# Kernel tuning notes

Measured on AMD Instinct MI355X. Metric: run time of the kernel, lower is better.

The kernel has to match this reference:

```python
import jax, jax.numpy as jnp
import numpy as np

DIM, HEADS, HD, TOPK, SCALE = 256, 8, 32, 4, 2


def _conv1x1(x, w, b):
    # 1x1 Conv2d with folded (eval-mode) BatchNorm -> affine: weight (O,C), bias (O,)
    return jnp.einsum('bchw,oc->bohw', x, w) + b[None, :, None, None]


def setup_inputs() -> dict:
    key = jax.random.key(0)
    ks = jax.random.split(key, 12)
    b, h, w = 2, 64, 64
    hu, wu = 32, 32
    s = lambda fan: 1.0 / np.sqrt(fan)
    return {
        'x': jax.random.normal(ks[0], (b, DIM, h, w), jnp.float32),
        'upper_feat': jax.random.normal(ks[1], (b, DIM, hu, wu), jnp.float32),
        'q_w': jax.random.normal(ks[2], (DIM, DIM), jnp.float32) * s(DIM),
        'q_b': jnp.zeros((DIM,), jnp.float32),
        'kv_w': jax.random.normal(ks[3], (2 * DIM, DIM), jnp.float32) * s(DIM),
        'kv_b': jnp.zeros((2 * DIM,), jnp.float32),
        'proj_w': jax.random.normal(ks[4], (DIM, DIM), jnp.float32) * s(DIM),
        'proj_b': jnp.zeros((DIM,), jnp.float32),
        'pe_w': jax.random.normal(ks[5], (DIM, 1, 7, 7), jnp.float32) * s(49),
        'pe_b': jnp.zeros((DIM,), jnp.float32),
        'gate_w': jax.random.normal(ks[6], (HD, 2 * HD), jnp.float32) * s(2 * HD),
        'gate_b': jnp.zeros((HD,), jnp.float32),
    }


def reference(x, upper_feat, q_w, q_b, kv_w, kv_b, proj_w, proj_b, pe_w, pe_b, gate_w, gate_b):
    b, c, h, w = x.shape
    n = h * w
    _, _, hu, wu = upper_feat.shape
    nu = hu * wu
    # projections -> (b, H, seq, d)
    q = _conv1x1(x, q_w, q_b).reshape(b, HEADS, HD, n).transpose(0, 1, 3, 2)
    kv = _conv1x1(upper_feat, kv_w, kv_b).reshape(b, HEADS, 2 * HD, nu).transpose(0, 1, 3, 2)
    k, v = kv[..., :HD], kv[..., HD:]
    # coarse cross-attention (fine queries -> coarse keys)
    sim = jnp.einsum('bhnd,bhmd->bhnm', q, k) * (HD ** -0.5)  # [b,H,n,nu]
    attn = jax.nn.softmax(sim, axis=-1)
    coarse = jnp.einsum('bhnm,bhmd->bhnd', attn, v)
    # fine branch: gumbel top-k over coarse positions, gather 2x2 fine blocks
    f_kv = _conv1x1(x, kv_w, kv_b).reshape(b, HEADS, 2 * HD, n).transpose(0, 1, 3, 2)
    f_k, f_v = f_kv[..., :HD], f_kv[..., HD:]
    gsim = sim.mean(axis=2)  # [b,H,nu]
    gum = jax.random.gumbel(jax.random.key(42), gsim.shape, gsim.dtype)
    soft = jax.nn.softmax(gsim + gum, axis=-1)
    _, ti = jax.lax.top_k(soft, TOPK)  # [b,H,k]
    h_idx = (ti // wu) * SCALE
    w_idx = (ti % wu) * SCALE
    txi = jnp.concatenate([(h_idx + dh) * w + (w_idx + dw)
                           for dh in range(SCALE) for dw in range(SCALE)], axis=-1)  # [b,H,4k]
    tk = jnp.take_along_axis(f_k, txi[..., None], axis=2)  # [b,H,4k,d]
    tv = jnp.take_along_axis(f_v, txi[..., None], axis=2)
    fine = jax.nn.softmax(jnp.einsum('bhnd,bhmd->bhnm', q, tk) * (HD ** -0.5), axis=-1)
    refined = jnp.einsum('bhnm,bhmd->bhnd', fine, tv)
    # gated fusion (Conv1d kernel_size=1 == linear over channels, shared across heads)
    fus = jnp.concatenate([coarse, refined], axis=-1)  # [b,H,n,2d]
    gate = jax.nn.sigmoid(jnp.einsum('bhnc,dc->bhnd', fus, gate_w) + gate_b)
    x_out = gate * refined + (1.0 - gate) * coarse
    x_out = x_out.transpose(0, 1, 3, 2).reshape(b, c, h, w)
    # depthwise 7x7 conv PE on coarse V, upsampled bilinearly (align_corners=False)
    v_r = v.transpose(0, 1, 3, 2).reshape(b, c, hu, wu)
    v_pe = jax.lax.conv_general_dilated(
        v_r, pe_w, window_strides=(1, 1), padding=((3, 3), (3, 3)),
        dimension_numbers=('NCHW', 'OIHW', 'NCHW'), feature_group_count=c)
    v_pe = v_pe + pe_b[None, :, None, None]
    v_pe = jax.image.resize(v_pe, (b, c, h, w), method='bilinear')
    return _conv1x1(x_out + v_pe, proj_w, proj_b)
```

## Files before the change

kernel.cpp:

```cpp
#include <hip/hip_runtime.h>
#include <cstdint>
#include <cstddef>

#define SCALE_F 0.17677669529663687f
#define SHIFT_F 8.0f

typedef __bf16 bf16x8 __attribute__((ext_vector_type(8)));
typedef float  floatx4 __attribute__((ext_vector_type(4)));
#define MFMA16(a,b,c) __builtin_amdgcn_mfma_f32_16x16x32_bf16(a, b, c, 0, 0, 0)

__device__ __forceinline__ unsigned short f2bf(float x) {
  unsigned u = __float_as_uint(x);
  u += 0x7FFFu + ((u >> 16) & 1u);
  return (unsigned short)(u >> 16);
}
__device__ __forceinline__ float bf2f(unsigned short h) {
  return __uint_as_float((unsigned)h << 16);
}
union bfu { unsigned short u; __bf16 b; };
__device__ __forceinline__ __bf16 us2bf(unsigned short u) { bfu t; t.u = u; return t.b; }
__device__ __forceinline__ void bfsplit(float x, unsigned short& h, unsigned short& l) {
  h = f2bf(x);
  l = f2bf(x - bf2f(h));
}
__device__ __forceinline__ unsigned cvt_pk_bf16(float lo, float hi) {
  unsigned r;
  asm("v_cvt_pk_bf16_f32 %0, %1, %2" : "=v"(r) : "v"(lo), "v"(hi));
  return r;
}
__device__ __forceinline__ void bfsplit2(float a, float b,
                                         unsigned& h2, unsigned& l2) {
  h2 = cvt_pk_bf16(a, b);
  float ra = a - __uint_as_float(h2 << 16);
  float rb = b - __uint_as_float(h2 & 0xffff0000u);
  l2 = cvt_pk_bf16(ra, rb);
}

__device__ __forceinline__ unsigned rotl32(unsigned v, int d) {
  return (v << d) | (v >> (32 - d));
}

__device__ __forceinline__ void threefry2x32(unsigned k0, unsigned k1,
                                             unsigned& x0, unsigned& x1) {
  unsigned k2 = k0 ^ k1 ^ 0x1BD11BDAu;
  x0 += k0; x1 += k1;
#define TF_R(r) { x0 += x1; x1 = rotl32(x1, r); x1 ^= x0; }
  TF_R(13) TF_R(15) TF_R(26) TF_R(6)
  x0 += k1; x1 += k2 + 1u;
  TF_R(17) TF_R(29) TF_R(16) TF_R(24)
  x0 += k2; x1 += k0 + 2u;
  TF_R(13) TF_R(15) TF_R(26) TF_R(6)
  x0 += k0; x1 += k1 + 3u;
  TF_R(17) TF_R(29) TF_R(16) TF_R(24)
  x0 += k1; x1 += k2 + 4u;
  TF_R(13) TF_R(15) TF_R(26) TF_R(6)
  x0 += k2; x1 += k0 + 5u;
#undef TF_R
}

__device__ __forceinline__ float jax_gumbel_key42(unsigned idx) {
  unsigned x0 = 0u, x1 = idx;
  threefry2x32(0u, 42u, x0, x1);
  unsigned bits = x0 ^ x1;
  unsigned fb = (bits >> 9) | 0x3f800000u;
  float f = __uint_as_float(fb) - 1.0f;
  const float tiny = 1.17549435e-38f;
  float u = f * (1.0f - tiny) + tiny;
  u = fmaxf(tiny, u);
  return -logf(-logf(u));
}

__device__ __forceinline__ float quad_xor1_add(float x) {
  int v = __builtin_amdgcn_mov_dpp(__float_as_int(x), 0xB1, 0xF, 0xF, true);
  return x + __int_as_float(v);
}
__device__ __forceinline__ float quad_xor2_add(float x) {
  int v = __builtin_amdgcn_mov_dpp(__float_as_int(x), 0x4E, 0xF, 0xF, true);
  return x + __int_as_float(v);
}

template<int MODE>
__device__ __forceinline__ void convmf_body(
    int bx, int by, int bz,
    const float* __restrict__ W, const float* __restrict__ bias,
    const float* __restrict__ X, float* __restrict__ Y,
    const float* __restrict__ vpe, float* __restrict__ qbar_g,
    unsigned short* __restrict__ bhs, unsigned short* __restrict__ bls) {
  const int tid  = threadIdx.x;
  const int lane = tid & 63;
  const int w    = tid >> 6;
  const int col  = lane & 15;
  const int quad = lane >> 4;
  const int sn0 = (tid & 15) * 4;
  const int sc0 = (tid >> 4) * 2;

  float wy0 = 0.f, wy1 = 0.f; int r0 = 0, r1 = 0;
  float wx0[4], wx1[4]; int cl0[4], cl1[4];
  if constexpr (MODE == 1) {
    float sy = 0.5f * (float)bx - 0.25f;
    int fy = (int)floorf(sy);
    wy1 = sy - (float)fy; wy0 = 1.0f - wy1;
    r0 = fy < 0 ? 0 : fy; r1 = (fy + 1) > 31 ? 31 : (fy + 1);
    #pragma unroll
    for (int k = 0; k < 4; ++k) {
      int jc = sn0 + k;
      float sx = 0.5f * (float)jc - 0.25f;
      int fx = (int)floorf(sx);
      wx1[k] = sx - (float)fx; wx0[k] = 1.0f - wx1[k];
      cl0[k] = fx < 0 ? 0 : fx; cl1[k] = (fx + 1) > 31 ? 31 : (fx + 1);
    }
  }

  const float* Xb = X + (size_t)bz * 256 * 4096 + bx * 64;

  bf16x8 wah[8], wal[8];
  {
    const float* wrow = W + (size_t)(by*64 + w*16 + col) * 256;
    #pragma unroll
    for (int s = 0; s < 8; ++s) {
      #pragma unroll
      for (int t = 0; t < 4; ++t) {
        float wa = wrow[s*32 + quad*8 + 2*t];
        float wb = wrow[s*32 + quad*8 + 2*t + 1];
        unsigned h2, l2;
        bfsplit2(wa, wb, h2, l2);
        ((unsigned*)&wah[s])[t] = h2;
        ((unsigned*)&wal[s])[t] = l2;
      }
    }
  }

  floatx4 f[4] = {{0.f,0.f,0.f,0.f},{0.f,0.f,0.f,0.f},{0.f,0.f,0.f,0.f},{0.f,0.f,0.f,0.f}};

  #pragma unroll
  for (int h2i = 0; h2i < 2; ++h2i) {
    #pragma unroll
    for (int s4 = 0; s4 < 4; ++s4) {
      int c = h2i*128 + s4*32 + sc0;
      int cl_ = c - h2i*128;
      float4 xa = *(const float4*)(Xb + (size_t)c * 4096 + sn0);
      float4 xb = *(const float4*)(Xb + (size_t)(c + 1) * 4096 + sn0);
      float ea[4] = {xa.x, xa.y, xa.z, xa.w};
      float eb[4] = {xb.x, xb.y, xb.z, xb.w};
      if constexpr (MODE == 1) {
        const float* vpa = vpe + ((size_t)bz * 256 + c) * 1024;
        const float* vpb = vpa + 1024;
        #pragma unroll
        for (int i = 0; i < 4; ++i) {
          ea[i] += wy0 * (wx0[i]*vpa[r0*32 + cl0[i]] + wx1[i]*vpa[r0*32 + cl1[i]])
                 + wy1 * (wx0[i]*vpa[r1*32 + cl0[i]] + wx1[i]*vpa[r1*32 + cl1[i]]);
          eb[i] += wy0 * (wx0[i]*vpb[r0*32 + cl0[i]] + wx1[i]*vpb[r0*32 + cl1[i]])
                 + wy1 * (wx0[i]*vpb[r1*32 + cl0[i]] + wx1[i]*vpb[r1*32 + cl1[i]]);
        }
      }
      #pragma unroll
      for (int i = 0; i < 4; ++i) {
        unsigned h2, l2;
        bfsplit2(ea[i], eb[i], h2, l2);
        *(unsigned*)(bhs + (sn0 + i) * 136 + cl_) = h2;
        *(unsigned*)(bls + (sn0 + i) * 136 + cl_) = l2;
      }
    }
    __syncthreads();

    #pragma unroll
    for (int sl = 0; sl < 4; ++sl) {
      int s = h2i*4 + sl;
      #pragma unroll
      for (int nt = 0; nt < 4; ++nt) {
        bf16x8 bh8 = *(const bf16x8*)(bhs + (nt*16 + col)*136 + sl*32 + quad*8);
        bf16x8 bl8 = *(const bf16x8*)(bls + (nt*16 + col)*136 + sl*32 + quad*8);
        f[nt] = MFMA16(wah[s], bh8, f[nt]);
        f[nt] = MFMA16(wal[s], bh8, f[nt]);
        f[nt] = MFMA16(wah[s], bl8, f[nt]);
      }
    }
    __syncthreads();
  }

  float* Yb = Y + (size_t)bz * 256 * 4096 + bx * 64;
  #pragma unroll
  for (int r = 0; r < 4; ++r) {
    int o = by*64 + w*16 + quad*4 + r;
    float bi = bias[o];
    float rs = 0.f;
    #pragma unroll
    for (int nt = 0; nt < 4; ++nt) {
      float val = f[nt][r] + bi;
      Yb[(size_t)o*4096 + nt*16 + col] = val;
      rs += val;
    }
    if constexpr (MODE == 0) {
      rs += __shfl_xor(rs, 1); rs += __shfl_xor(rs, 2);
      rs += __shfl_xor(rs, 4); rs += __shfl_xor(rs, 8);
      if (col == 0) atomicAdd(qbar_g + bz*256 + o, rs);
    }
  }
}

__device__ __forceinline__ void convkv_body(
    int bx, int by, int bz,
    const float* __restrict__ W, const float* __restrict__ bias,
    const float* __restrict__ X, float* __restrict__ Y,
    float* __restrict__ Y2,
    unsigned short* __restrict__ KH, unsigned short* __restrict__ KL,
    unsigned short* __restrict__ VH, unsigned short* __restrict__ VL,
    float (*As)[68], float (*Bs)[68]) {
  const int tid = threadIdx.x;
  const int tx = tid & 15, ty = tid >> 4;
  const int C = 256, N = 1024;
  const float* Xb = X + (size_t)bz * C * N + bx * 64;
  const int ar = tid >> 2;
  const int ac = (tid & 3) * 4;
  const int bc = tid >> 4;
  const int bn = (tid & 15) * 4;
  float acc[4][4] = {};

  for (int kc = 0; kc < C; kc += 32) {
    float4 av0 = *(const float4*)(W + (size_t)(by * 64 + ar) * C + kc + ac);
    float4 av1 = *(const float4*)(W + (size_t)(by * 64 + ar) * C + kc + 16 + ac);
    float4 bv0 = *(const float4*)(Xb + (size_t)(kc + bc) * N + bn);
    float4 bv1 = *(const float4*)(Xb + (size_t)(kc + 16 + bc) * N + bn);
    As[ac+0][ar]  = av0.x; As[ac+1][ar]  = av0.y; As[ac+2][ar]  = av0.z; As[ac+3][ar]  = av0.w;
    As[ac+16][ar] = av1.x; As[ac+17][ar] = av1.y; As[ac+18][ar] = av1.z; As[ac+19][ar] = av1.w;
    *(float4*)&Bs[bc][bn]      = bv0;
    *(float4*)&Bs[bc + 16][bn] = bv1;
    __syncthreads();
    #pragma unroll 8
    for (int kk = 0; kk < 32; ++kk) {
      float4 a = *(const float4*)&As[kk][ty*4];
      float4 b = *(const float4*)&Bs[kk][tx*4];
      acc[0][0] = fmaf(a.x, b.x, acc[0][0]); acc[0][1] = fmaf(a.x, b.y, acc[0][1]);
      acc[0][2] = fmaf(a.x, b.z, acc[0][2]); acc[0][3] = fmaf(a.x, b.w, acc[0][3]);
      acc[1][0] = fmaf(a.y, b.x, acc[1][0]); acc[1][1] = fmaf(a.y, b.y, acc[1][1]);
      acc[1][2] = fmaf(a.y, b.z, acc[1][2]); acc[1][3] = fmaf(a.y, b.w, acc[1][3]);
      acc[2][0] = fmaf(a.z, b.x, acc[2][0]); acc[2][1] = fmaf(a.z, b.y, acc[2][1]);
      acc[2][2] = fmaf(a.z, b.z, acc[2][2]); acc[2][3] = fmaf(a.z, b.w, acc[2][3]);
      acc[3][0] = fmaf(a.w, b.x, acc[3][0]); acc[3][1] = fmaf(a.w, b.y, acc[3][1]);
      acc[3][2] = fmaf(a.w, b.z, acc[3][2]); acc[3][3] = fmaf(a.w, b.w, acc[3][3]);
    }
    __syncthreads();
  }

  float vals[4][4];
  #pragma unroll
  for (int i = 0; i < 4; ++i) {
    float bi = bias[by*64 + ty*4 + i];
    #pragma unroll
    for (int j = 0; j < 4; ++j) vals[i][j] = acc[i][j] + bi;
  }

  #pragma unroll
  for (int i = 0; i < 4; ++i) {
    int o = by*64 + ty*4 + i;
    int hh = o >> 6, dd = o & 63;
    float* yb = Y + (size_t)bz*524288 + (size_t)hh*65536 + dd;
    #pragma unroll
    for (int j = 0; j < 4; ++j) {
      int m = bx*64 + tx*4 + j;
      yb[(size_t)m*64] = vals[i][j];
      if (dd >= 32)
        Y2[((size_t)bz*256 + hh*32 + (dd-32))*1024 + m] = vals[i][j];
    }
  }
  const int bh_ = bz*8 + by;
  const int dd0 = ty*4;
  if (dd0 < 32) {
    #pragma unroll
    for (int j = 0; j < 4; ++j) {
      int m = bx*64 + tx*4 + j;
      uint2 ph, pl;
      bfsplit2(vals[0][j], vals[1][j], ph.x, pl.x);
      bfsplit2(vals[2][j], vals[3][j], ph.y, pl.y);
      *(uint2*)(KH + ((size_t)bh_*1024 + m)*32 + dd0) = ph;
      *(uint2*)(KL + ((size_t)bh_*1024 + m)*32 + dd0) = pl;
    }
  } else {
    const int m0 = bx*64 + tx*4;
    const int ml = (m0 >> 2) & 7;
    const int mp = (m0 & ~31) + ((ml & 3) << 3) + ((ml >> 2) << 2);
    #pragma unroll
    for (int i = 0; i < 4; ++i) {
      int dv = dd0 + i - 32;
      uint2 ph, pl;
      bfsplit2(vals[i][0], vals[i][1], ph.x, pl.x);
      bfsplit2(vals[i][2], vals[i][3], ph.y, pl.y);
      *(uint2*)(VH + ((size_t)bh_*32 + dv)*1024 + mp) = ph;
      *(uint2*)(VL + ((size_t)bh_*32 + dv)*1024 + mp) = pl;
    }
  }
}

__global__ __launch_bounds__(256)
void front_kernel(const float* __restrict__ q_w, const float* __restrict__ q_b,
                  const float* __restrict__ x, float* __restrict__ q_cm,
                  float* __restrict__ qbar_g,
                  const float* __restrict__ kv_w, const float* __restrict__ kv_b,
                  const float* __restrict__ upper,
                  float* __restrict__ kv_m, float* __restrict__ v_ch,
                  unsigned short* __restrict__ KH, unsigned short* __restrict__ KL,
                  unsigned short* __restrict__ VH, unsigned short* __restrict__ VL) {
  __shared__ __align__(16) char fsm[34816];
  if (blockIdx.x < 256) {
    int idx = blockIdx.x;
    convkv_body(idx & 15, (idx >> 4) & 7, idx >> 7,
                kv_w, kv_b, upper, kv_m, v_ch, KH, KL, VH, VL,
                (float(*)[68])fsm, (float(*)[68])(fsm + 8704));
  } else {
    int idx = blockIdx.x - 256;
    convmf_body<0>(idx & 63, (idx >> 6) & 3, idx >> 8,
                   q_w, q_b, x, q_cm, nullptr, qbar_g,
                   (unsigned short*)fsm, (unsigned short*)(fsm + 17408));
  }
}

__global__ __launch_bounds__(256)
void mid_kernel(const float* __restrict__ qbar_g, const float* __restrict__ kv_m,
                const float* __restrict__ x, const float* __restrict__ kv_w,
                const float* __restrict__ kv_b, float* __restrict__ fkv_g,
                const float* __restrict__ v_ch, const float* __restrict__ pe_w,
                const float* __restrict__ pe_b, float* __restrict__ v_pe) {
  __shared__ float qbar[32];
  __shared__ float vals[1024];
  __shared__ float rv[256];
  __shared__ int ri[256];
  __shared__ int txi_s[16];
  __shared__ float xcol[16][260];
  __shared__ float vch[1024];
  __shared__ float wch[49];
  const int tid = threadIdx.x;

  if (blockIdx.x < 64) {
    const int bh = blockIdx.x >> 2;
    const int quarter = blockIdx.x & 3;
    const int b = bh >> 3, hh = bh & 7;

    if (tid < 32) qbar[tid] = qbar_g[b*256 + hh*32 + tid] * (1.0f/4096.0f);
    __syncthreads();

    for (int m = tid; m < 1024; m += 256) {
      const float* kbp = kv_m + (size_t)bh*65536 + (size_t)m*64;
      float s = 0.f;
      #pragma unroll
      for (int d4 = 0; d4 < 8; ++d4) {
        float4 kk = *(const float4*)&kbp[d4*4];
        s = fmaf(qbar[d4*4+0], kk.x, s);
        s = fmaf(qbar[d4*4+1], kk.y, s);
        s = fmaf(qbar[d4*4+2], kk.z, s);
        s = fmaf(qbar[d4*4+3], kk.w, s);
      }
      vals[m] = s * SCALE_F + jax_gumbel_key42((unsigned)(bh*1024 + m));
    }
    __syncthreads();

    int sel[4];
    for (int t = 0; t < 4; ++t) {
      float bv = -INFINITY; int bi = 0x7fffffff;
      for (int m = tid; m < 1024; m += 256) {
        float v = vals[m];
        if (v > bv || (v == bv && m < bi)) { bv = v; bi = m; }
      }
      rv[tid] = bv; ri[tid] = bi;
      __syncthreads();
      for (int st = 128; st >= 1; st >>= 1) {
        if (tid < st) {
          float ov = rv[tid+st]; int oi = ri[tid+st];
          if (ov > rv[tid] || (ov == rv[tid] && oi < ri[tid])) { rv[tid] = ov; ri[tid] = oi; }
        }
        __syncthreads();
      }
      int w = ri[0];
      sel[t] = w;
      __syncthreads();
      if (tid == 0) vals[w] = -INFINITY;
      __syncthreads();
    }

    if (tid == 0) {
      #pragma unroll
      for (int t = 0; t < 4; ++t) {
        int ti = sel[t];
        int hi = (ti >> 5) * 2, wi = (ti & 31) * 2;
        #pragma unroll
        for (int dh = 0; dh < 2; ++dh)
          #pragma unroll
          for (int dw = 0; dw < 2; ++dw)
            txi_s[(dh*2+dw)*4 + t] = (hi+dh)*64 + (wi+dw);
      }
    }
    __syncthreads();

    #pragma unroll
    for (int i = 0; i < 16; ++i) {
      int e = tid + 256*i;
      int c = e >> 4, j = e & 15;
      xcol[j][c] = x[(size_t)b*1048576 + (size_t)c*4096 + txi_s[j]];
    }
    __syncthreads();
    const int dd = quarter*16 + (tid >> 4);
    const int j  = tid & 15;
    const int o  = hh*64 + dd;
    const float* wrow = kv_w + (size_t)o*256;
    float a0 = 0.f, a1 = 0.f, a2 = 0.f, a3 = 0.f;
    const float* xc = &xcol[j][0];
    #pragma unroll 4
    for (int c = 0; c < 256; c += 4) {
      a0 = fmaf(wrow[c+0], xc[c+0], a0);
      a1 = fmaf(wrow[c+1], xc[c+1], a1);
      a2 = fmaf(wrow[c+2], xc[c+2], a2);
      a3 = fmaf(wrow[c+3], xc[c+3], a3);
    }
    fkv_g[(size_t)bh*1024 + dd*16 + j] = ((a0+a1)+(a2+a3)) + kv_b[o];
  } else {
    const int bc = blockIdx.x - 64;
    const int b = bc >> 8, c = bc & 255;
    const float* src = v_ch + ((size_t)b*256 + c)*1024;
    #pragma unroll
    for (int i = 0; i < 4; ++i) vch[tid + 256*i] = src[tid + 256*i];
    if (tid < 49) wch[tid] = pe_w[c*49 + tid];
    float pb = pe_b[c];
    __syncthreads();
    #pragma unroll
    for (int pi = 0; pi < 4; ++pi) {
      int p = tid + 256*pi;
      int i0 = p >> 5, j0 = p & 31;
      float s = 0.f;
      #pragma unroll
      for (int ky = 0; ky < 7; ++ky) {
        int yy = i0 + ky - 3;
        if (yy < 0 || yy > 31) continue;
        #pragma unroll
        for (int kx = 0; kx < 7; ++kx) {
          int xx = j0 + kx - 3;
          if (xx < 0 || xx > 31) continue;
          s = fmaf(wch[ky*7+kx], vch[yy*32+xx], s);
        }
      }
      v_pe[((size_t)b*256 + c)*1024 + p] = s + pb;
    }
  }
}

__global__ __launch_bounds__(256)
void proj_kernel(const float* __restrict__ proj_w, const float* __restrict__ proj_b,
                 const float* __restrict__ x_o, float* __restrict__ out,
                 const float* __restrict__ vpe) {
  __shared__ __align__(16) char fsm[34816];
  convmf_body<1>(blockIdx.x, blockIdx.y, blockIdx.z,
                 proj_w, proj_b, x_o, out, vpe, nullptr,
                 (unsigned short*)fsm, (unsigned short*)(fsm + 17408));
}

__global__ __launch_bounds__(512, 2)
void attn_kernel(const float* __restrict__ q_cm,
                 const unsigned short* __restrict__ kb_h,
                 const unsigned short* __restrict__ kb_l,
                 const unsigned short* __restrict__ vb_h,
                 const unsigned short* __restrict__ vb_l,
                 const float* __restrict__ fkv_g,
                 const float* __restrict__ gate_w, const float* __restrict__ gate_b,
                 float* __restrict__ x_o) {
  __shared__ __align__(16) char smem[48256];
  float* gw_s = (float*)smem;
  float* gb_s = (float*)(smem + 9216);
  float* tk   = (float*)(smem + 9344);
  float* tv   = (float*)(smem + 11392);
  char*  region = smem + 13440;

  const int tid  = threadIdx.x;
  const int lane = tid & 63;
  const int w    = tid >> 6;
  const int qpair = w & 3;
  const int half  = w >> 2;
  const int col  = lane & 15;
  const int quad = lane >> 4;

  const int linear = blockIdx.y * 32 + blockIdx.x;
  const int xcd  = linear & 7;
  const int slot = linear >> 3;
  const int bh = xcd * 2 + (slot >> 5);
  const int nx = slot & 31;
  const int b = bh >> 3, hh = bh & 7;
  const int n0 = nx * 128;

  #pragma unroll
  for (int i = 0; i < 4; ++i) {
    int e = tid + 512*i;
    gw_s[(e >> 6)*72 + (e & 63)] = gate_w[e];
  }
  if (tid < 32) gb_s[tid] = gate_b[tid];

  if (tid < 256) {
    const float* src = fkv_g + (size_t)bh * 1024;
    #pragma unroll
    for (int i = 0; i < 4; ++i) {
      int e4 = (tid & 63) + 64 * i;
      float4 val = ((const float4*)src)[e4];
      int e = e4 * 4;
      int dd = e >> 4, j0 = e & 15;
      float* dst = (dd < 32) ? tk : tv;
      int ddv = (dd < 32) ? dd : dd - 32;
      dst[(j0+0)*32 + ddv] = val.x;
      dst[(j0+1)*32 + ddv] = val.y;
      dst[(j0+2)*32 + ddv] = val.z;
      dst[(j0+3)*32 + ddv] = val.w;
    }
  }
  __syncthreads();

  const float* qbase_cm = q_cm + ((size_t)b*256 + hh*32)*4096 + n0;
  const int qf = tid >> 2;
  const int sf = tid & 3;

  bf16x8 aqh0, aql0, aqh1, aql1;
  #pragma unroll
  for (int j = 0; j < 8; ++j) {
    float qv0 = qbase_cm[(size_t)(quad*8 + j)*4096 + qpair*32 + col];
    float qv1 = qbase_cm[(size_t)(quad*8 + j)*4096 + qpair*32 + 16 + col];
    unsigned short h, l;
    bfsplit(qv0, h, l);
    aqh0[j] = us2bf(h); aql0[j] = us2bf(l);
    bfsplit(qv1, h, l);
    aqh1[j] = us2bf(h); aql1[j] = us2bf(l);
  }

  const unsigned short* kph = kb_h + (size_t)bh * 32768;
  const unsigned short* kpl = kb_l + (size_t)bh * 32768;
  const unsigned short* vph = vb_h + (size_t)bh * 32768;
  const unsigned short* vpl = vb_l + (size_t)bh * 32768;
  const int mbase = half * 512;

#define LDKH(c, t) (*(const bf16x8*)(kph + ((size_t)(mbase + (c)*32 + (t)*16 + col))*32 + quad*8))
#define LDKL(c, t) (*(const bf16x8*)(kpl + ((size_t)(mbase + (c)*32 + (t)*16 + col))*32 + quad*8))
#define LDVH(c, t) (*(const bf16x8*)(vph + ((size_t)((t)*16 + col))*1024 + mbase + (c)*32 + quad*8))
#define LDVL(c, t) (*(const bf16x8*)(vpl + ((size_t)((t)*16 + col))*1024 + mbase + (c)*32 + quad*8))

  floatx4 oA0 = {0.f,0.f,0.f,0.f}, oA1 = {0.f,0.f,0.f,0.f};
  floatx4 oB0 = {0.f,0.f,0.f,0.f}, oB1 = {0.f,0.f,0.f,0.f};
  const floatx4 zero = {0.f, 0.f, 0.f, 0.f};
  float lsA = 0.f, lsB = 0.f;

  floatx4 sA0, sA1, sB0, sB1;
  {
    bf16x8 k0h = LDKH(0,0), k1h = LDKH(0,1);
    bf16x8 k0l = LDKL(0,0), k1l = LDKL(0,1);
    sA0 = MFMA16(k0h, aqh0, zero); sA0 = MFMA16(k0h, aql0, sA0); sA0 = MFMA16(k0l, aqh0, sA0);
    sA1 = MFMA16(k1h, aqh0, zero); sA1 = MFMA16(k1h, aql0, sA1); sA1 = MFMA16(k1l, aqh0, sA1);
    sB0 = MFMA16(k0h, aqh1, zero); sB0 = MFMA16(k0h, aql1, sB0); sB0 = MFMA16(k0l, aqh1, sB0);
    sB1 = MFMA16(k1h, aqh1, zero); sB1 = MFMA16(k1h, aql1, sB1); sB1 = MFMA16(k1l, aqh1, sB1);
  }

  for (int c = 0; c < 16; ++c) {
    bf16x8 v0h = LDVH(c,0), v1h = LDVH(c,1);
    bf16x8 v0l = LDVL(c,0), v1l = LDVL(c,1);
    bf16x8 nk0h, nk1h, nk0l, nk1l;
    if (c < 15) {
      nk0h = LDKH(c+1,0); nk1h = LDKH(c+1,1);
      nk0l = LDKL(c+1,0); nk1l = LDKL(c+1,1);
    }

    float pA0[4], pA1[4], pB0[4], pB1[4];
    #pragma unroll
    for (int r = 0; r < 4; ++r) {
      pA0[r] = __expf(fmaf(sA0[r], SCALE_F, -SHIFT_F));
      pA1[r] = __expf(fmaf(sA1[r], SCALE_F, -SHIFT_F));
      pB0[r] = __expf(fmaf(sB0[r], SCALE_F, -SHIFT_F));
      pB1[r] = __expf(fmaf(sB1[r], SCALE_F, -SHIFT_F));
      lsA += pA0[r] + pA1[r];
      lsB += pB0[r] + pB1[r];
    }
    bf16x8 paA, paB;
    ((unsigned*)&paA)[0] = cvt_pk_bf16(pA0[0], pA0[1]);
    ((unsigned*)&paA)[1] = cvt_pk_bf16(pA0[2], pA0[3]);
    ((unsigned*)&paA)[2] = cvt_pk_bf16(pA1[0], pA1[1]);
    ((unsigned*)&paA)[3] = cvt_pk_bf16(pA1[2], pA1[3]);
    ((unsigned*)&paB)[0] = cvt_pk_bf16(pB0[0], pB0[1]);
    ((unsigned*)&paB)[1] = cvt_pk_bf16(pB0[2], pB0[3]);
    ((unsigned*)&paB)[2] = cvt_pk_bf16(pB1[0], pB1[1]);
    ((unsigned*)&paB)[3] = cvt_pk_bf16(pB1[2], pB1[3]);

    oA0 = MFMA16(paA, v0h, oA0); oA0 = MFMA16(paA, v0l, oA0);
    oA1 = MFMA16(paA, v1h, oA1); oA1 = MFMA16(paA, v1l, oA1);
    oB0 = MFMA16(paB, v0h, oB0); oB0 = MFMA16(paB, v0l, oB0);
    oB1 = MFMA16(paB, v1h, oB1); oB1 = MFMA16(paB, v1l, oB1);

    if (c < 15) {
      sA0 = MFMA16(nk0h, aqh0, zero); sA0 = MFMA16(nk0h, aql0, sA0); sA0 = MFMA16(nk0l, aqh0, sA0);
      sA1 = MFMA16(nk1h, aqh0, zero); sA1 = MFMA16(nk1h, aql0, sA1); sA1 = MFMA16(nk1l, aqh0, sA1);
      sB0 = MFMA16(nk0h, aqh1, zero); sB0 = MFMA16(nk0h, aql1, sB0); sB0 = MFMA16(nk0l, aqh1, sB0);
      sB1 = MFMA16(nk1h, aqh1, zero); sB1 = MFMA16(nk1h, aql1, sB1); sB1 = MFMA16(nk1l, aqh1, sB1);
    }
  }
#undef LDKH
#undef LDKL
#undef LDVH
#undef LDVL

  lsA += __shfl_xor(lsA, 16); lsA += __shfl_xor(lsA, 32);
  lsB += __shfl_xor(lsB, 16); lsB += __shfl_xor(lsB, 32);

  {
    float* cacc = (float*)region;
    float* cl   = (float*)region + 8448;
    #pragma unroll
    for (int r = 0; r < 4; ++r) {
      int qa = qpair*32 + quad*4 + r;
      cacc[(half*128 + qa)*33 + col]      = oA0[r];
      cacc[(half*128 + qa)*33 + 16 + col] = oA1[r];
      int qb = qa + 16;
      cacc[(half*128 + qb)*33 + col]      = oB0[r];
      cacc[(half*128 + qb)*33 + 16 + col] = oB1[r];
    }
    if (quad == 0) {
      cl[half*128 + qpair*32 + col]      = lsA;
      cl[half*128 + qpair*32 + 16 + col] = lsB;
    }
  }

  float rfn[8];
  float crs[8];
  {
    float qfv[8];
    #pragma unroll
    for (int j = 0; j < 8; ++j)
      qfv[j] = qbase_cm[(size_t)(sf + 4*j)*4096 + qf];
    float p16[16]; float fl = 0.f;
    #pragma unroll
    for (int k = 0; k < 16; ++k) {
      const float* kr = tk + k*32 + sf;
      float tp = qfv[0]*kr[0];
      tp = fmaf(qfv[1], kr[4], tp);  tp = fmaf(qfv[2], kr[8], tp);
      tp = fmaf(qfv[3], kr[12], tp); tp = fmaf(qfv[4], kr[16], tp);
      tp = fmaf(qfv[5], kr[20], tp); tp = fmaf(qfv[6], kr[24], tp);
      tp = fmaf(qfv[7], kr[28], tp);
      float full = quad_xor2_add(quad_xor1_add(tp));
      float e = __expf(fmaf(full, SCALE_F, -SHIFT_F));
      p16[k] = e; fl += e;
    }
    float finv = 1.0f / fl;
    #pragma unroll
    for (int j = 0; j < 8; ++j) {
      float r = 0.f;
      #pragma unroll
      for (int k = 0; k < 16; ++k) r = fmaf(p16[k], tv[k*32 + sf + 4*j], r);
      rfn[j] = r * finv;
    }
  }
  __syncthreads();

  {
    const float* cacc = (const float*)region;
    const float* cl   = (const float*)region + 8448;
    float lt = cl[qf] + cl[128 + qf];
    float cinv = 1.0f / lt;
    #pragma unroll
    for (int j = 0; j < 8; ++j) {
      int d = sf + 4*j;
      crs[j] = (cacc[qf*33 + d] + cacc[(128 + qf)*33 + d]) * cinv;
    }
  }
  __syncthreads();

  {
    float* fus = (float*)region;
    #pragma unroll
    for (int j = 0; j < 8; ++j) {
      fus[qf*68 + sf + 4*j]      = crs[j];
      fus[qf*68 + 32 + sf + 4*j] = rfn[j];
    }
  }
  __syncthreads();

  {
    const float* fus = (const float*)region + qf*68;
    float ga[8];
    #pragma unroll
    for (int j = 0; j < 8; ++j) ga[j] = gb_s[sf + 4*j];
    #pragma unroll
    for (int c4 = 0; c4 < 16; ++c4) {
      float4 fv = *(const float4*)(fus + c4*4);
      #pragma unroll
      for (int j = 0; j < 8; ++j) {
        float4 wv = *(const float4*)(gw_s + (sf + 4*j)*72 + c4*4);
        ga[j] = fmaf(wv.x, fv.x, fmaf(wv.y, fv.y, fmaf(wv.z, fv.z, fmaf(wv.w, fv.w, ga[j]))));
      }
    }
    float* xob = x_o + ((size_t)b*256 + hh*32)*4096 + n0 + qf;
    #pragma unroll
    for (int j = 0; j < 8; ++j) {
      float g = 1.0f / (1.0f + __expf(-ga[j]));
      xob[(size_t)(sf + 4*j)*4096] = g*rfn[j] + (1.0f - g)*crs[j];
    }
  }
}

extern "C" void kernel_launch(void* const* d_in, const int* in_sizes, int n_in,
                              void* d_out, int out_size, void* d_ws, size_t ws_size,
                              hipStream_t stream) {
  const float* x      = (const float*)d_in[0];
  const float* upper  = (const float*)d_in[1];
  const float* q_w    = (const float*)d_in[2];
  const float* q_b    = (const float*)d_in[3];
  const float* kv_w   = (const float*)d_in[4];
  const float* kv_b   = (const float*)d_in[5];
  const float* proj_w = (const float*)d_in[6];
  const float* proj_b = (const float*)d_in[7];
  const float* pe_w   = (const float*)d_in[8];
  const float* pe_b   = (const float*)d_in[9];
  const float* gate_w = (const float*)d_in[10];
  const float* gate_b = (const float*)d_in[11];
  float* out = (float*)d_out;
  float* ws  = (float*)d_ws;

  float* q_cm  = ws;
  float* kv_m  = q_cm + 2097152;
  float* v_ch  = kv_m + 1048576;
  float* x_o   = v_ch + 524288;
  float* v_pe  = x_o  + 2097152;
  float* fkv_g = v_pe + 524288;
  float* qbar_g = fkv_g + 16384;
  unsigned short* kb_h = (unsigned short*)(qbar_g + 512);
  unsigned short* kb_l = kb_h + 524288;
  unsigned short* vb_h = kb_l + 524288;
  unsigned short* vb_l = vb_h + 524288;

  hipMemsetAsync(qbar_g, 0, 512 * sizeof(float), stream);

  front_kernel<<<dim3(768), 256, 0, stream>>>(
      q_w, q_b, x, q_cm, qbar_g,
      kv_w, kv_b, upper, kv_m, v_ch, kb_h, kb_l, vb_h, vb_l);
  mid_kernel<<<dim3(576), 256, 0, stream>>>(
      qbar_g, kv_m, x, kv_w, kv_b, fkv_g, v_ch, pe_w, pe_b, v_pe);
  attn_kernel<<<dim3(32, 16), 512, 0, stream>>>(
      q_cm, kb_h, kb_l, vb_h, vb_l, fkv_g, gate_w, gate_b, x_o);
  proj_kernel<<<dim3(64, 4, 2), 256, 0, stream>>>(
      proj_w, proj_b, x_o, out, v_pe);
}
```

Before: 207.1 us.

## Compute query mean via channel sums of x and move Q projection to mid kernel

The mean of Q over positions is now obtained algebraically as q_w times the per-channel spatial mean of x plus q_b, computed by lightweight reduction blocks in the front kernel. The full Q projection no longer has to finish before top-k selection, so it moves into the mid kernel alongside the top-k and PE blocks. This shortens the critical path and the front kernel's shared memory use. In exchange x is read one extra time, mid_kernel grows to more blocks with a larger shared allocation, and the mean is now summed in a different order.

```diff
diff --git a/kernel.cpp b/kernel.cpp
--- a/kernel.cpp
+++ b/kernel.cpp
@@ -84,7 +84,7 @@
     int bx, int by, int bz,
     const float* __restrict__ W, const float* __restrict__ bias,
     const float* __restrict__ X, float* __restrict__ Y,
-    const float* __restrict__ vpe, float* __restrict__ qbar_g,
+    const float* __restrict__ vpe,
     unsigned short* __restrict__ bhs, unsigned short* __restrict__ bls) {
   const int tid  = threadIdx.x;
   const int lane = tid & 63;
@@ -183,17 +183,9 @@
   for (int r = 0; r < 4; ++r) {
     int o = by*64 + w*16 + quad*4 + r;
     float bi = bias[o];
-    float rs = 0.f;
     #pragma unroll
     for (int nt = 0; nt < 4; ++nt) {
-      float val = f[nt][r] + bi;
-      Yb[(size_t)o*4096 + nt*16 + col] = val;
-      rs += val;
-    }
-    if constexpr (MODE == 0) {
-      rs += __shfl_xor(rs, 1); rs += __shfl_xor(rs, 2);
-      rs += __shfl_xor(rs, 4); rs += __shfl_xor(rs, 8);
-      if (col == 0) atomicAdd(qbar_g + bz*256 + o, rs);
+      Yb[(size_t)o*4096 + nt*16 + col] = f[nt][r] + bi;
     }
   }
 }
@@ -292,50 +284,74 @@
 }
 
 __global__ __launch_bounds__(256)
-void front_kernel(const float* __restrict__ q_w, const float* __restrict__ q_b,
-                  const float* __restrict__ x, float* __restrict__ q_cm,
-                  float* __restrict__ qbar_g,
+void front_kernel(const float* __restrict__ q_w,
+                  const float* __restrict__ x, float* __restrict__ qbar_g,
                   const float* __restrict__ kv_w, const float* __restrict__ kv_b,
                   const float* __restrict__ upper,
                   float* __restrict__ kv_m, float* __restrict__ v_ch,
                   unsigned short* __restrict__ KH, unsigned short* __restrict__ KL,
                   unsigned short* __restrict__ VH, unsigned short* __restrict__ VL) {
-  __shared__ __align__(16) char fsm[34816];
+  __shared__ __align__(16) char fsm[17408];
+  const int tid = threadIdx.x;
   if (blockIdx.x < 256) {
     int idx = blockIdx.x;
     convkv_body(idx & 15, (idx >> 4) & 7, idx >> 7,
                 kv_w, kv_b, upper, kv_m, v_ch, KH, KL, VH, VL,
                 (float(*)[68])fsm, (float(*)[68])(fsm + 8704));
   } else {
-    int idx = blockIdx.x - 256;
-    convmf_body<0>(idx & 63, (idx >> 6) & 3, idx >> 8,
-                   q_w, q_b, x, q_cm, nullptr, qbar_g,
-                   (unsigned short*)fsm, (unsigned short*)(fsm + 17408));
+    int p = blockIdx.x - 256;
+    int b = p >> 8, c = p & 255;
+    float* red = (float*)fsm;
+    const float* xr = x + ((size_t)b*256 + c)*4096;
+    float s = 0.f;
+    #pragma unroll
+    for (int i = 0; i < 4; ++i) {
+      float4 v = *(const float4*)(xr + (tid + 256*i) * 4);
+      s += (v.x + v.y) + (v.z + v.w);
+    }
+    red[tid] = s;
+    __syncthreads();
+    for (int st = 128; st >= 1; st >>= 1) {
+      if (tid < st) red[tid] += red[tid + st];
+      __syncthreads();
+    }
+    float xs = red[0];
+    atomicAdd(qbar_g + b*256 + tid, q_w[(size_t)tid*256 + c] * xs);
   }
 }
 
 __global__ __launch_bounds__(256)
-void mid_kernel(const float* __restrict__ qbar_g, const float* __restrict__ kv_m,
-                const float* __restrict__ x, const float* __restrict__ kv_w,
-                const float* __restrict__ kv_b, float* __restrict__ fkv_g,
+void mid_kernel(const float* __restrict__ q_w, const float* __restrict__ q_b,
+                const float* __restrict__ x, float* __restrict__ q_cm,
+                const float* __restrict__ qbar_g, const float* __restrict__ kv_m,
+                const float* __restrict__ kv_w, const float* __restrict__ kv_b,
+                float* __restrict__ fkv_g,
                 const float* __restrict__ v_ch, const float* __restrict__ pe_w,
                 const float* __restrict__ pe_b, float* __restrict__ v_pe) {
-  __shared__ float qbar[32];
-  __shared__ float vals[1024];
-  __shared__ float rv[256];
-  __shared__ int ri[256];
-  __shared__ int txi_s[16];
-  __shared__ float xcol[16][260];
-  __shared__ float vch[1024];
-  __shared__ float wch[49];
+  __shared__ __align__(16) char fsm[34816];
   const int tid = threadIdx.x;
 
+  if (blockIdx.x >= 64 && blockIdx.x < 576) {
+    int idx = blockIdx.x - 64;
+    convmf_body<0>(idx & 63, (idx >> 6) & 3, idx >> 8,
+                   q_w, q_b, x, q_cm, nullptr,
+                   (unsigned short*)fsm, (unsigned short*)(fsm + 17408));
+    return;
+  }
+
   if (blockIdx.x < 64) {
+    float* qbar = (float*)fsm;
+    float* vals = (float*)(fsm + 128);
+    float* rv   = (float*)(fsm + 4224);
+    int*   ri   = (int*)(fsm + 5248);
+    int*   txi_s= (int*)(fsm + 6272);
+    float (*xcol)[260] = (float(*)[260])(fsm + 6336);
     const int bh = blockIdx.x >> 2;
     const int quarter = blockIdx.x & 3;
     const int b = bh >> 3, hh = bh & 7;
 
-    if (tid < 32) qbar[tid] = qbar_g[b*256 + hh*32 + tid] * (1.0f/4096.0f);
+    if (tid < 32)
+      qbar[tid] = qbar_g[b*256 + hh*32 + tid] * (1.0f/4096.0f) + q_b[hh*32 + tid];
     __syncthreads();
 
     for (int m = tid; m < 1024; m += 256) {
@@ -412,7 +428,9 @@
     }
     fkv_g[(size_t)bh*1024 + dd*16 + j] = ((a0+a1)+(a2+a3)) + kv_b[o];
   } else {
-    const int bc = blockIdx.x - 64;
+    float* vch = (float*)fsm;
+    float* wch = (float*)(fsm + 4096);
+    const int bc = blockIdx.x - 576;
     const int b = bc >> 8, c = bc & 255;
     const float* src = v_ch + ((size_t)b*256 + c)*1024;
     #pragma unroll
@@ -447,7 +465,7 @@
                  const float* __restrict__ vpe) {
   __shared__ __align__(16) char fsm[34816];
   convmf_body<1>(blockIdx.x, blockIdx.y, blockIdx.z,
-                 proj_w, proj_b, x_o, out, vpe, nullptr,
+                 proj_w, proj_b, x_o, out, vpe,
                  (unsigned short*)fsm, (unsigned short*)(fsm + 17408));
 }
 
@@ -727,10 +745,11 @@
   hipMemsetAsync(qbar_g, 0, 512 * sizeof(float), stream);
 
   front_kernel<<<dim3(768), 256, 0, stream>>>(
-      q_w, q_b, x, q_cm, qbar_g,
+      q_w, x, qbar_g,
       kv_w, kv_b, upper, kv_m, v_ch, kb_h, kb_l, vb_h, vb_l);
-  mid_kernel<<<dim3(576), 256, 0, stream>>>(
-      qbar_g, kv_m, x, kv_w, kv_b, fkv_g, v_ch, pe_w, pe_b, v_pe);
+  mid_kernel<<<dim3(1088), 256, 0, stream>>>(
+      q_w, q_b, x, q_cm, qbar_g, kv_m, kv_w, kv_b, fkv_g,
+      v_ch, pe_w, pe_b, v_pe);
   attn_kernel<<<dim3(32, 16), 512, 0, stream>>>(
       q_cm, kb_h, kb_l, vb_h, vb_l, fkv_g, gate_w, gate_b, x_o);
   proj_kernel<<<dim3(64, 4, 2), 256, 0, stream>>>(
```

Result: no change. 206.5 us (median of 2 runs) (-0.3%).
